# Optimization experiments

Hardware: AMD Instinct MI355X
Metric: run time of the kernel (lower is better)

The kernel has to match this reference:

```python
import jax, jax.numpy as jnp
import numpy as np

N = 100000      # nodes
R = 4           # relations
E = 500000      # edges per relation
IN, HID, OUT = 128, 128, 64


def _rel_conv(x, src, dst, W, b):
    """One DGL GraphConv (norm='both') over one relation's edge list.
    out = D_dst^{-1/2} * segsum_dst( D_src^{-1/2} x[src] ) @ W + b
    """
    ones = jnp.ones(src.shape[0], dtype=x.dtype)
    out_deg = jax.ops.segment_sum(ones, src, num_segments=N)
    in_deg = jax.ops.segment_sum(ones, dst, num_segments=N)
    norm_src = jax.lax.rsqrt(jnp.maximum(out_deg, 1.0))
    norm_dst = jax.lax.rsqrt(jnp.maximum(in_deg, 1.0))
    msg = (x * norm_src[:, None])[src]                       # [E, d] gather
    agg = jax.ops.segment_sum(msg, dst, num_segments=N)      # [N, d] scatter-add
    agg = agg * norm_dst[:, None]
    return agg @ W + b


def setup_inputs() -> dict:
    key = jax.random.key(0)
    ks = jax.random.split(key, 8)
    x = jax.random.normal(ks[0], (N, IN), dtype=jnp.float32)
    edge_src = jax.random.randint(ks[1], (R, E), 0, N, dtype=jnp.int32)
    edge_dst = jax.random.randint(ks[2], (R, E), 0, N, dtype=jnp.int32)
    s1 = 1.0 / np.sqrt(IN)
    s2 = 1.0 / np.sqrt(HID)
    W1 = jax.random.normal(ks[3], (R, IN, HID), dtype=jnp.float32) * s1
    b1 = jnp.zeros((R, HID), dtype=jnp.float32)
    W2 = jax.random.normal(ks[4], (R, HID, OUT), dtype=jnp.float32) * s2
    b2 = jnp.zeros((R, OUT), dtype=jnp.float32)
    return {"x": x, "edge_src": edge_src, "edge_dst": edge_dst,
            "W1": W1, "b1": b1, "W2": W2, "b2": b2}


def reference(x, edge_src, edge_dst, W1, b1, W2, b2):
    # layer 1: per-relation GraphConv, aggregate='sum' across relations
    h = _rel_conv(x, edge_src[0], edge_dst[0], W1[0], b1[0])
    for r in range(1, R):
        h = h + _rel_conv(x, edge_src[r], edge_dst[r], W1[r], b1[r])
    h = jax.nn.relu(h)
    # layer 2
    out = _rel_conv(h, edge_src[0], edge_dst[0], W2[0], b2[0])
    for r in range(1, R):
        out = out + _rel_conv(h, edge_src[r], edge_dst[r], W2[r], b2[r])
    return out
```

## Files before the change

kernel.cpp:

```cpp
#include <hip/hip_runtime.h>


constexpr int Nn  = 100000;
constexpr int Rr  = 4;
constexpr int Ee  = 500000;
constexpr int RE  = Rr * Ee;
constexpr int TOT = Rr * Nn;
constexpr int NP  = 100096;
constexpr int NPB = NP / 128;
constexpr int CAPN = 56;

constexpr int CB2   = (RE / 2 + 255) / 256;
constexpr int GB1   = 4 * NPB;
constexpr int PAIR1 = 2 * GB1;
constexpr int P1_GRID = PAIR1 + (CB2 - GB1) + 1;

constexpr int FB = (RE / 4 + 255) / 256;

typedef short bf16x8 __attribute__((ext_vector_type(8)));
typedef float f32x4  __attribute__((ext_vector_type(4)));

__device__ __forceinline__ unsigned short f2bf(float f) {
    unsigned u = __builtin_bit_cast(unsigned, f);
    u = u + 0x7FFFu + ((u >> 16) & 1u);
    return (unsigned short)(u >> 16);
}
__device__ __forceinline__ float bf2f(unsigned short h) {
    unsigned u = ((unsigned)h) << 16;
    return __builtin_bit_cast(float, u);
}
__device__ __forceinline__ float bfbits_lo(unsigned p) {
    return __builtin_bit_cast(float, p << 16);
}
__device__ __forceinline__ float bfbits_hi(unsigned p) {
    return __builtin_bit_cast(float, p & 0xFFFF0000u);
}

__device__ __forceinline__ void count_body2(int sub, int tid,
    const int* __restrict__ src, const int* __restrict__ dst,
    unsigned* __restrict__ deg, unsigned* __restrict__ slot)
{
    int e0 = (sub * 256 + tid) * 2;
    if (e0 >= RE) return;
    int r = (unsigned)e0 / (unsigned)Ee;
    int base = r * Nn;
    int2 s2 = *reinterpret_cast<const int2*>(src + e0);
    int2 d2 = *reinterpret_cast<const int2*>(dst + e0);
    atomicAdd(&deg[base + s2.x], 1u);
    atomicAdd(&deg[base + s2.y], 1u);
    uint2 sl;
    sl.x = atomicAdd(&deg[TOT + d2.x * Rr + r], 1u);
    sl.y = atomicAdd(&deg[TOT + d2.y * Rr + r], 1u);
    *reinterpret_cast<uint2*>(slot + e0) = sl;
}

__device__ __forceinline__ void bsum_body(int tid,
    const float* __restrict__ b1, const float* __restrict__ b2,
    float* __restrict__ bs1, float* __restrict__ bs2)
{
    if (tid < 128) bs1[tid] = b1[tid] + b1[128 + tid] + b1[256 + tid] + b1[384 + tid];
    if (tid < 64)  bs2[tid] = b2[tid] + b2[64 + tid] + b2[128 + tid] + b2[192 + tid];
}

template<int BN, bool CONVA, bool ALO>
__device__ __forceinline__ void gemm_body(
    const short* __restrict__ Xh, const short* __restrict__ Xl,
    const float* __restrict__ Xf,
    const short* __restrict__ WhT_, const short* __restrict__ WlT_,
    short* __restrict__ Y_, int CW, int rowblk, int rel)
{
    constexpr int BM = 128, BKp = 40;
    constexpr int MFR = (BN == 128) ? 4 : 2;
    constexpr int NFR = 4;
    const short* WhT = WhT_ + (size_t)rel * (BN * 128);
    const short* WlT = WlT_ + (size_t)rel * (BN * 128);
    short* Y = Y_ + (size_t)rel * BN;

    __shared__ __align__(16) short Ah[BM * BKp];
    __shared__ __align__(16) short Al[ALO ? BM * BKp : 16];
    __shared__ __align__(16) short Bh[BN * BKp], Bl[BN * BKp];

    const int tid = threadIdx.x;
    const int lane = tid & 63, wid = tid >> 6;
    const int lr = lane & 15, lg = lane >> 4;
    const int wm0 = (BN == 128) ? (wid >> 1) * 64 : wid * 32;
    const int wn0 = (BN == 128) ? (wid & 1) * 64 : 0;
    const int row0 = rowblk * BM;

    f32x4 acc[MFR][NFR];
    #pragma unroll
    for (int m = 0; m < MFR; ++m)
        #pragma unroll
        for (int n = 0; n < NFR; ++n)
            #pragma unroll
            for (int j = 0; j < 4; ++j) acc[m][n][j] = 0.f;

    const int sr = tid >> 1;
    const int sko = (tid & 1) * 16;

    for (int ks = 0; ks < 4; ++ks) {
        if constexpr (CONVA) {
            int grow = row0 + sr;
            float v[16];
            if (grow < Nn) {
                const float* xp = Xf + (size_t)grow * 128 + ks * 32 + sko;
                float4 a0 = *reinterpret_cast<const float4*>(xp);
                float4 a1 = *reinterpret_cast<const float4*>(xp + 4);
                float4 a2 = *reinterpret_cast<const float4*>(xp + 8);
                float4 a3 = *reinterpret_cast<const float4*>(xp + 12);
                v[0]=a0.x; v[1]=a0.y; v[2]=a0.z; v[3]=a0.w;
                v[4]=a1.x; v[5]=a1.y; v[6]=a1.z; v[7]=a1.w;
                v[8]=a2.x; v[9]=a2.y; v[10]=a2.z; v[11]=a2.w;
                v[12]=a3.x; v[13]=a3.y; v[14]=a3.z; v[15]=a3.w;
            } else {
                #pragma unroll
                for (int i = 0; i < 16; ++i) v[i] = 0.f;
            }
            bf16x8 h0, h1, l0, l1;
            #pragma unroll
            for (int i = 0; i < 8; ++i) {
                unsigned short h = f2bf(v[i]);
                h0[i] = (short)h; l0[i] = (short)f2bf(v[i] - bf2f(h));
                unsigned short g = f2bf(v[8 + i]);
                h1[i] = (short)g; l1[i] = (short)f2bf(v[8 + i] - bf2f(g));
            }
            *reinterpret_cast<bf16x8*>(&Ah[sr * BKp + sko])     = h0;
            *reinterpret_cast<bf16x8*>(&Ah[sr * BKp + sko + 8]) = h1;
            *reinterpret_cast<bf16x8*>(&Al[sr * BKp + sko])     = l0;
            *reinterpret_cast<bf16x8*>(&Al[sr * BKp + sko + 8]) = l1;
        } else {
            size_t ga = (size_t)(row0 + sr) * 128 + ks * 32 + sko;
            *reinterpret_cast<bf16x8*>(&Ah[sr * BKp + sko])     = *reinterpret_cast<const bf16x8*>(&Xh[ga]);
            *reinterpret_cast<bf16x8*>(&Ah[sr * BKp + sko + 8]) = *reinterpret_cast<const bf16x8*>(&Xh[ga + 8]);
            if constexpr (ALO) {
                *reinterpret_cast<bf16x8*>(&Al[sr * BKp + sko])     = *reinterpret_cast<const bf16x8*>(&Xl[ga]);
                *reinterpret_cast<bf16x8*>(&Al[sr * BKp + sko + 8]) = *reinterpret_cast<const bf16x8*>(&Xl[ga + 8]);
            }
        }
        if (BN == 128 || tid < 128) {
            size_t gb = (size_t)sr * 128 + ks * 32 + sko;
            *reinterpret_cast<bf16x8*>(&Bh[sr * BKp + sko])     = *reinterpret_cast<const bf16x8*>(&WhT[gb]);
            *reinterpret_cast<bf16x8*>(&Bh[sr * BKp + sko + 8]) = *reinterpret_cast<const bf16x8*>(&WhT[gb + 8]);
            *reinterpret_cast<bf16x8*>(&Bl[sr * BKp + sko])     = *reinterpret_cast<const bf16x8*>(&WlT[gb]);
            *reinterpret_cast<bf16x8*>(&Bl[sr * BKp + sko + 8]) = *reinterpret_cast<const bf16x8*>(&WlT[gb + 8]);
        }
        __syncthreads();

        bf16x8 bh[NFR], bl[NFR];
        #pragma unroll
        for (int n = 0; n < NFR; ++n) {
            bh[n] = *reinterpret_cast<const bf16x8*>(&Bh[(wn0 + n * 16 + lr) * BKp + lg * 8]);
            bl[n] = *reinterpret_cast<const bf16x8*>(&Bl[(wn0 + n * 16 + lr) * BKp + lg * 8]);
        }
        __builtin_amdgcn_s_setprio(1);
        #pragma unroll
        for (int m = 0; m < MFR; ++m) {
            bf16x8 ah = *reinterpret_cast<const bf16x8*>(&Ah[(wm0 + m * 16 + lr) * BKp + lg * 8]);
            #pragma unroll
            for (int n = 0; n < NFR; ++n) {
                acc[m][n] = __builtin_amdgcn_mfma_f32_16x16x32_bf16(ah, bh[n], acc[m][n], 0, 0, 0);
                acc[m][n] = __builtin_amdgcn_mfma_f32_16x16x32_bf16(ah, bl[n], acc[m][n], 0, 0, 0);
            }
            if constexpr (ALO) {
                bf16x8 al = *reinterpret_cast<const bf16x8*>(&Al[(wm0 + m * 16 + lr) * BKp + lg * 8]);
                #pragma unroll
                for (int n = 0; n < NFR; ++n)
                    acc[m][n] = __builtin_amdgcn_mfma_f32_16x16x32_bf16(al, bh[n], acc[m][n], 0, 0, 0);
            }
        }
        __builtin_amdgcn_s_setprio(0);
        __syncthreads();
    }

    #pragma unroll
    for (int m = 0; m < MFR; ++m)
        #pragma unroll
        for (int n = 0; n < NFR; ++n) {
            int col = wn0 + n * 16 + lr;
            int rb = row0 + wm0 + m * 16 + lg * 4;
            #pragma unroll
            for (int j = 0; j < 4; ++j)
                Y[(size_t)(rb + j) * CW + col] = (short)f2bf(acc[m][n][j]);
        }
}

__global__ __launch_bounds__(256)
void phase1_kernel(const int* __restrict__ src, const int* __restrict__ dst,
                   unsigned* __restrict__ deg, unsigned* __restrict__ slot,
                   const float* __restrict__ X,
                   const short* __restrict__ w1h, const short* __restrict__ w1l,
                   short* __restrict__ Y,
                   const float* __restrict__ b1, const float* __restrict__ b2,
                   float* __restrict__ bs1, float* __restrict__ bs2)
{
    int bid = blockIdx.x, tid = threadIdx.x;
    if (bid < PAIR1) {
        int sub = bid >> 1;
        if (bid & 1) {
            int rel = sub & 3, rowblk = sub >> 2;
            gemm_body<128, true, true>(nullptr, nullptr, X, w1h, w1l, Y, 512, rowblk, rel);
        } else {
            count_body2(sub, tid, src, dst, deg, slot);
        }
    } else {
        int t = bid - PAIR1;
        if (t < CB2 - GB1) count_body2(GB1 + t, tid, src, dst, deg, slot);
        else              bsum_body(tid, b1, b2, bs1, bs2);
    }
}

__global__ __launch_bounds__(256)
void count_kernel(const int* __restrict__ src, const int* __restrict__ dst,
                  unsigned* __restrict__ deg, unsigned* __restrict__ slot)
{
    count_body2(blockIdx.x, threadIdx.x, src, dst, deg, slot);
}

__global__ void bsum_kernel(const float* __restrict__ b1, const float* __restrict__ b2,
                            float* __restrict__ bs1, float* __restrict__ bs2)
{
    bsum_body(threadIdx.x, b1, b2, bs1, bs2);
}

__global__ __launch_bounds__(256)
void norms_kernel(const unsigned* __restrict__ deg, float* __restrict__ nsrc,
                  uint4* __restrict__ degq, float4* __restrict__ ndstq)
{
    int gid = blockIdx.x * 256 + threadIdx.x;
    if (gid < TOT) {
        unsigned sd = deg[gid];
        nsrc[gid] = rsqrtf((float)(sd > 0u ? sd : 1u));
    }
    if (gid < Nn) {
        uint4 dq = *reinterpret_cast<const uint4*>(deg + TOT + gid * 4);
        degq[gid] = dq;
        float4 nq;
        nq.x = rsqrtf((float)(dq.x > 0u ? dq.x : 1u));
        nq.y = rsqrtf((float)(dq.y > 0u ? dq.y : 1u));
        nq.z = rsqrtf((float)(dq.z > 0u ? dq.z : 1u));
        nq.w = rsqrtf((float)(dq.w > 0u ? dq.w : 1u));
        ndstq[gid] = nq;
    }
}

__global__ __launch_bounds__(256)
void fill_csr_kernel(const int* __restrict__ src, const int* __restrict__ dst,
                     const unsigned* __restrict__ slot, const uint4* __restrict__ degq,
                     const float4* __restrict__ ndstq, const float* __restrict__ nsrc,
                     int2* __restrict__ csrw)
{
    int e0 = (blockIdx.x * 256 + threadIdx.x) * 4;
    if (e0 >= RE) return;
    int r = (unsigned)e0 / (unsigned)Ee;
    int base = r * Nn;
    int4 s4 = *reinterpret_cast<const int4*>(src + e0);
    int4 d4 = *reinterpret_cast<const int4*>(dst + e0);
    uint4 sl = *reinterpret_cast<const uint4*>(slot + e0);
    #pragma unroll
    for (int i = 0; i < 4; ++i) {
        int s = (i == 0) ? s4.x : (i == 1) ? s4.y : (i == 2) ? s4.z : s4.w;
        int d = (i == 0) ? d4.x : (i == 1) ? d4.y : (i == 2) ? d4.z : d4.w;
        unsigned k = (i == 0) ? sl.x : (i == 1) ? sl.y : (i == 2) ? sl.z : sl.w;
        uint4 dq = degq[d];
        float4 nq = ndstq[d];
        unsigned pre = (r > 0 ? dq.x : 0u) + (r > 1 ? dq.y : 0u) + (r > 2 ? dq.z : 0u);
        float nd = (r == 0) ? nq.x : (r == 1) ? nq.y : (r == 2) ? nq.z : nq.w;
        float w = nsrc[base + s] * nd;
        unsigned pos = pre + k;
        if (pos < (unsigned)CAPN) {
            int2 v; v.x = s | (r << 17); v.y = __builtin_bit_cast(int, w);
            csrw[(size_t)d * CAPN + pos] = v;
        }
    }
}

__global__ __launch_bounds__(256)
void convw_kernel(const float* __restrict__ W1, const float* __restrict__ W2,
                  short* __restrict__ w1h, short* __restrict__ w1l,
                  short* __restrict__ w2h, short* __restrict__ w2l)
{
    int gid = blockIdx.x * 256 + threadIdx.x;
    if (gid < 4 * 128 * 128) {
        int r = gid >> 14, rem = gid & 16383, n = rem >> 7, k = rem & 127;
        float v = W1[(r << 14) + k * 128 + n];
        unsigned short h = f2bf(v);
        unsigned short l = f2bf(v - bf2f(h));
        w1h[(r << 14) + n * 128 + k] = (short)h;
        w1l[(r << 14) + n * 128 + k] = (short)l;
    } else {
        int g2 = gid - 65536;
        if (g2 >= 4 * 64 * 128) return;
        int r = g2 >> 13, rem = g2 & 8191, n = rem >> 7, k = rem & 127;
        float v = W2[(r << 13) + k * 64 + n];
        unsigned short h = f2bf(v);
        unsigned short l = f2bf(v - bf2f(h));
        w2h[(r << 13) + n * 128 + k] = (short)h;
        w2l[(r << 13) + n * 128 + k] = (short)l;
    }
}

template<int BN, bool CONVA, bool ALO>
__global__ __launch_bounds__(256)
void gemm_kernel(const short* __restrict__ Xh, const short* __restrict__ Xl,
                 const float* __restrict__ Xf,
                 const short* __restrict__ WhT_, const short* __restrict__ WlT_,
                 short* __restrict__ Y_, int CW)
{
    gemm_body<BN, CONVA, ALO>(Xh, Xl, Xf, WhT_, WlT_, Y_, CW, blockIdx.x, blockIdx.y);
}

__global__ __launch_bounds__(512)
void gemm64f_kernel(const short* __restrict__ Xh,
                    const short* __restrict__ w2h, const short* __restrict__ w2l,
                    short* __restrict__ Y)
{
    constexpr int BKp = 40;
    __shared__ __align__(16) short Ah[128 * BKp];
    __shared__ __align__(16) short Bh[256 * BKp], Bl[256 * BKp];

    const int tid = threadIdx.x;
    const int lane = tid & 63, wv = tid >> 6;
    const int rel = wv >> 1, wm0 = (wv & 1) * 64;
    const int lr = lane & 15, lg = lane >> 4;
    const int row0 = blockIdx.x * 128;

    f32x4 acc[4][4];
    #pragma unroll
    for (int m = 0; m < 4; ++m)
        #pragma unroll
        for (int n = 0; n < 4; ++n)
            #pragma unroll
            for (int j = 0; j < 4; ++j) acc[m][n][j] = 0.f;

    const int sra = tid >> 2, ska = (tid & 3) * 8;
    const int rb = tid >> 7, nb = (tid >> 1) & 63, skb = (tid & 1) * 16;

    for (int ks = 0; ks < 4; ++ks) {
        size_t ga = (size_t)(row0 + sra) * 128 + ks * 32 + ska;
        *reinterpret_cast<bf16x8*>(&Ah[sra * BKp + ska]) = *reinterpret_cast<const bf16x8*>(&Xh[ga]);
        size_t gb = (size_t)rb * (64 * 128) + (size_t)nb * 128 + ks * 32 + skb;
        *reinterpret_cast<bf16x8*>(&Bh[(rb * 64 + nb) * BKp + skb])     = *reinterpret_cast<const bf16x8*>(&w2h[gb]);
        *reinterpret_cast<bf16x8*>(&Bh[(rb * 64 + nb) * BKp + skb + 8]) = *reinterpret_cast<const bf16x8*>(&w2h[gb + 8]);
        *reinterpret_cast<bf16x8*>(&Bl[(rb * 64 + nb) * BKp + skb])     = *reinterpret_cast<const bf16x8*>(&w2l[gb]);
        *reinterpret_cast<bf16x8*>(&Bl[(rb * 64 + nb) * BKp + skb + 8]) = *reinterpret_cast<const bf16x8*>(&w2l[gb + 8]);
        __syncthreads();

        bf16x8 bh[4], bl[4];
        #pragma unroll
        for (int n = 0; n < 4; ++n) {
            bh[n] = *reinterpret_cast<const bf16x8*>(&Bh[(rel * 64 + n * 16 + lr) * BKp + lg * 8]);
            bl[n] = *reinterpret_cast<const bf16x8*>(&Bl[(rel * 64 + n * 16 + lr) * BKp + lg * 8]);
        }
        __builtin_amdgcn_s_setprio(1);
        #pragma unroll
        for (int m = 0; m < 4; ++m) {
            bf16x8 ah = *reinterpret_cast<const bf16x8*>(&Ah[(wm0 + m * 16 + lr) * BKp + lg * 8]);
            #pragma unroll
            for (int n = 0; n < 4; ++n) {
                acc[m][n] = __builtin_amdgcn_mfma_f32_16x16x32_bf16(ah, bh[n], acc[m][n], 0, 0, 0);
                acc[m][n] = __builtin_amdgcn_mfma_f32_16x16x32_bf16(ah, bl[n], acc[m][n], 0, 0, 0);
            }
        }
        __builtin_amdgcn_s_setprio(0);
        __syncthreads();
    }

    #pragma unroll
    for (int m = 0; m < 4; ++m)
        #pragma unroll
        for (int n = 0; n < 4; ++n) {
            int col = rel * 64 + n * 16 + lr;
            int rbse = row0 + wm0 + m * 16 + lg * 4;
            #pragma unroll
            for (int j = 0; j < 4; ++j)
                Y[(size_t)(rbse + j) * 256 + col] = (short)f2bf(acc[m][n][j]);
        }
}

template<int F, int NRl>
__global__ __launch_bounds__(256)
void gather_kernel(const short* __restrict__ Y, const uint4* __restrict__ degq,
                   const int2* __restrict__ csrw, const float* __restrict__ bsum,
                   float* __restrict__ H, short* __restrict__ Xh,
                   int CW, int rel, int accumulate, int finalize)
{
    constexpr int LPE = (F == 128) ? 16 : 8;
    constexpr int QN  = 64 / LPE;
    constexpr int FL  = F / LPE;
    int wid = (blockIdx.x * 256 + threadIdx.x) >> 6;
    int lane = threadIdx.x & 63;
    int q = lane / LPE, li = lane & (LPE - 1);
    if (wid >= Nn) return;

    uint4 dq = degq[wid];
    unsigned e, e1;
    if (NRl == 4) {
        unsigned tot = dq.x + dq.y + dq.z + dq.w;
        if (tot > (unsigned)CAPN) tot = CAPN;
        e = (unsigned)wid * CAPN; e1 = e + tot;
    } else {
        unsigned pre = (rel > 0 ? dq.x : 0u) + (rel > 1 ? dq.y : 0u) + (rel > 2 ? dq.z : 0u);
        unsigned len = (rel == 0) ? dq.x : (rel == 1) ? dq.y : (rel == 2) ? dq.z : dq.w;
        if (pre > (unsigned)CAPN) pre = CAPN;
        if (pre + len > (unsigned)CAPN) len = CAPN - pre;
        e = (unsigned)wid * CAPN + pre; e1 = e + len;
    }

    float t[FL];
    #pragma unroll
    for (int f = 0; f < FL; ++f) t[f] = 0.f;

    auto yaddr = [&](int2 a) -> const short* {
        int s = a.x & 0x1FFFF;
        int rl = (NRl == 4) ? ((a.x >> 17) & 3) : 0;
        return Y + (size_t)s * CW + rl * F + li * FL;
    };
    auto accum1 = [&](int2 a) {
        const short* ya = yaddr(a);
        float wa = __builtin_bit_cast(float, a.y);
        uint4 pa = *reinterpret_cast<const uint4*>(ya);
        t[0] += wa * bfbits_lo(pa.x); t[1] += wa * bfbits_hi(pa.x);
        t[2] += wa * bfbits_lo(pa.y); t[3] += wa * bfbits_hi(pa.y);
        t[4] += wa * bfbits_lo(pa.z); t[5] += wa * bfbits_hi(pa.z);
        t[6] += wa * bfbits_lo(pa.w); t[7] += wa * bfbits_hi(pa.w);
    };

    for (; e + 4 * QN <= e1; e += 4 * QN) {
        int2 a0 = csrw[e + q], a1 = csrw[e + QN + q];
        int2 a2 = csrw[e + 2 * QN + q], a3 = csrw[e + 3 * QN + q];
        const short* y0 = yaddr(a0); const short* y1 = yaddr(a1);
        const short* y2 = yaddr(a2); const short* y3 = yaddr(a3);
        float w0 = __builtin_bit_cast(float, a0.y), w1 = __builtin_bit_cast(float, a1.y);
        float w2 = __builtin_bit_cast(float, a2.y), w3 = __builtin_bit_cast(float, a3.y);
        uint4 p0 = *reinterpret_cast<const uint4*>(y0);
        uint4 p1 = *reinterpret_cast<const uint4*>(y1);
        uint4 p2 = *reinterpret_cast<const uint4*>(y2);
        uint4 p3 = *reinterpret_cast<const uint4*>(y3);
        t[0] += w0*bfbits_lo(p0.x) + w1*bfbits_lo(p1.x) + w2*bfbits_lo(p2.x) + w3*bfbits_lo(p3.x);
        t[1] += w0*bfbits_hi(p0.x) + w1*bfbits_hi(p1.x) + w2*bfbits_hi(p2.x) + w3*bfbits_hi(p3.x);
        t[2] += w0*bfbits_lo(p0.y) + w1*bfbits_lo(p1.y) + w2*bfbits_lo(p2.y) + w3*bfbits_lo(p3.y);
        t[3] += w0*bfbits_hi(p0.y) + w1*bfbits_hi(p1.y) + w2*bfbits_hi(p2.y) + w3*bfbits_hi(p3.y);
        t[4] += w0*bfbits_lo(p0.z) + w1*bfbits_lo(p1.z) + w2*bfbits_lo(p2.z) + w3*bfbits_lo(p3.z);
        t[5] += w0*bfbits_hi(p0.z) + w1*bfbits_hi(p1.z) + w2*bfbits_hi(p2.z) + w3*bfbits_hi(p3.z);
        t[6] += w0*bfbits_lo(p0.w) + w1*bfbits_lo(p1.w) + w2*bfbits_lo(p2.w) + w3*bfbits_lo(p3.w);
        t[7] += w0*bfbits_hi(p0.w) + w1*bfbits_hi(p1.w) + w2*bfbits_hi(p2.w) + w3*bfbits_hi(p3.w);
    }
    if (e + 2 * QN <= e1) {
        int2 a0 = csrw[e + q], a1 = csrw[e + QN + q];
        const short* y0 = yaddr(a0); const short* y1 = yaddr(a1);
        float w0 = __builtin_bit_cast(float, a0.y), w1 = __builtin_bit_cast(float, a1.y);
        uint4 p0 = *reinterpret_cast<const uint4*>(y0);
        uint4 p1 = *reinterpret_cast<const uint4*>(y1);
        t[0] += w0*bfbits_lo(p0.x) + w1*bfbits_lo(p1.x);
        t[1] += w0*bfbits_hi(p0.x) + w1*bfbits_hi(p1.x);
        t[2] += w0*bfbits_lo(p0.y) + w1*bfbits_lo(p1.y);
        t[3] += w0*bfbits_hi(p0.y) + w1*bfbits_hi(p1.y);
        t[4] += w0*bfbits_lo(p0.z) + w1*bfbits_lo(p1.z);
        t[5] += w0*bfbits_hi(p0.z) + w1*bfbits_hi(p1.z);
        t[6] += w0*bfbits_lo(p0.w) + w1*bfbits_lo(p1.w);
        t[7] += w0*bfbits_hi(p0.w) + w1*bfbits_hi(p1.w);
        e += 2 * QN;
    }
    if (e + QN <= e1) {
        accum1(csrw[e + q]);
        e += QN;
    }
    int nrem = (int)(e1 - e);
    if (q < nrem) accum1(csrw[e + q]);

    #pragma unroll
    for (int f = 0; f < FL; ++f) {
        #pragma unroll
        for (int o = LPE; o < 64; o <<= 1)
            t[f] += __shfl_xor(t[f], o, 64);
    }
    if (q != 0) return;

    float* hp = H + (size_t)wid * F + li * FL;
    if (accumulate) {
        #pragma unroll
        for (int f = 0; f < FL; ++f) t[f] += hp[f];
    } else {
        #pragma unroll
        for (int f = 0; f < FL; ++f) t[f] += bsum[li * FL + f];
    }
    if (F == 128 && finalize) {
        short hv[8];
        #pragma unroll
        for (int f = 0; f < FL; ++f)
            hv[f] = (short)f2bf(fmaxf(t[f], 0.f));
        *reinterpret_cast<uint4*>(Xh + (size_t)wid * F + li * FL) = *reinterpret_cast<uint4*>(hv);
    } else {
        *reinterpret_cast<float4*>(hp)     = make_float4(t[0], t[1], t[2], t[3]);
        *reinterpret_cast<float4*>(hp + 4) = make_float4(t[4], t[5], t[6], t[7]);
    }
}

extern "C" void kernel_launch(void* const* d_in, const int* in_sizes, int n_in,
                              void* d_out, int out_size, void* d_ws, size_t ws_size,
                              hipStream_t stream)
{
    const float* x  = (const float*)d_in[0];
    const int* esrc = (const int*)d_in[1];
    const int* edst = (const int*)d_in[2];
    const float* W1 = (const float*)d_in[3];
    const float* b1 = (const float*)d_in[4];
    const float* W2 = (const float*)d_in[5];
    const float* b2 = (const float*)d_in[6];
    float* out = (float*)d_out;

    char* ws = (char*)d_ws;
    size_t off = 0;
    auto alloc = [&](size_t bytes) { char* p = ws + off; off += (bytes + 255) & ~(size_t)255; return p; };
    unsigned* deg   = (unsigned*)alloc((size_t)2 * TOT * 4);
    float*    nsrc  = (float*)   alloc((size_t)TOT * 4);
    uint4*    degq  = (uint4*)   alloc((size_t)Nn * 16);
    float4*   ndstq = (float4*)  alloc((size_t)Nn * 16);
    unsigned* slot  = (unsigned*)alloc((size_t)RE * 4);
    float*    bs1   = (float*)   alloc(128 * 4);
    float*    bs2   = (float*)   alloc(64 * 4);
    short*    w1h   = (short*)   alloc((size_t)4 * 128 * 128 * 2);
    short*    w1l   = (short*)   alloc((size_t)4 * 128 * 128 * 2);
    short*    w2h   = (short*)   alloc((size_t)4 * 64 * 128 * 2);
    short*    w2l   = (short*)   alloc((size_t)4 * 64 * 128 * 2);
    int2*     csrw  = (int2*)    alloc((size_t)Nn * CAPN * 8);
    short*    xh    = (short*)   alloc((size_t)NP * 128 * 2);

    size_t yslot = (size_t)NP * 128 * 2;
    bool pathA = (ws_size >= off + 4 * yslot + 4096);
    float* h = nullptr;
    short* Y;
    if (pathA) {
        Y = (short*)alloc(4 * yslot);
    } else {
        h = (float*)alloc((size_t)NP * 128 * 4);
        Y = (short*)alloc(yslot);
    }

    const int ggrid = (Nn * 64 + 255) / 256;
    const int ngrid = (TOT + 255) / 256;

    convw_kernel<<<384, 256, 0, stream>>>(W1, W2, w1h, w1l, w2h, w2l);
    hipMemsetAsync(deg, 0, (size_t)2 * TOT * 4, stream);

    if (pathA) {
        phase1_kernel<<<P1_GRID, 256, 0, stream>>>(
            esrc, edst, deg, slot, x, w1h, w1l, Y, b1, b2, bs1, bs2);
        norms_kernel<<<ngrid, 256, 0, stream>>>(deg, nsrc, degq, ndstq);
        fill_csr_kernel<<<FB, 256, 0, stream>>>(esrc, edst, slot, degq, ndstq, nsrc, csrw);
        gather_kernel<128, 4><<<ggrid, 256, 0, stream>>>(
            Y, degq, csrw, bs1, (float*)out , xh, 512, 0, 0, 1);
        gemm64f_kernel<<<NPB, 512, 0, stream>>>(xh, w2h, w2l, Y);
        gather_kernel<64, 4><<<ggrid, 256, 0, stream>>>(
            Y, degq, csrw, bs2, out, nullptr, 256, 0, 0, 0);
    } else {
        count_kernel<<<CB2, 256, 0, stream>>>(esrc, edst, deg, slot);
        bsum_kernel<<<1, 128, 0, stream>>>(b1, b2, bs1, bs2);
        norms_kernel<<<ngrid, 256, 0, stream>>>(deg, nsrc, degq, ndstq);
        fill_csr_kernel<<<FB, 256, 0, stream>>>(esrc, edst, slot, degq, ndstq, nsrc, csrw);
        for (int r = 0; r < Rr; ++r) {
            gemm_kernel<128, true, true><<<dim3(NPB, 1), 256, 0, stream>>>(
                nullptr, nullptr, x, w1h + (size_t)r * 128 * 128, w1l + (size_t)r * 128 * 128, Y, 128);
            gather_kernel<128, 1><<<ggrid, 256, 0, stream>>>(
                Y, degq, csrw, bs1, h, xh, 128, r, r > 0, r == Rr - 1);
        }
        for (int r = 0; r < Rr; ++r) {
            gemm_kernel<64, false, false><<<dim3(NPB, 1), 256, 0, stream>>>(
                xh, nullptr, nullptr, w2h + (size_t)r * 64 * 128, w2l + (size_t)r * 64 * 128, Y, 64);
            gather_kernel<64, 1><<<ggrid, 256, 0, stream>>>(
                Y, degq, csrw, bs2, out, nullptr, 64, r, r > 0, 0);
        }
    }
}
```

Before: 386.9 us.

## Fuse layer-1 gather with layer-2 GEMM and drop norms kernel

Removes the separate norms kernel: fill_csr now computes rsqrt of the source and destination degrees inline from the raw degree array, and gather reads the in-degree quads directly. It also adds a fused kernel that gathers the layer-1 aggregate for 128 rows into shared memory, applies bias and ReLU, and immediately runs the layer-2 MFMA GEMM. This avoids writing and re-reading the bf16 hidden matrix and saves kernel launches. In exchange it uses a large shared-memory footprint, which lowers occupancy for the latency-bound gather phase, and it needs a separate Y2 buffer when the workspace is large enough.

```diff
diff --git a/kernel.cpp b/kernel.cpp
--- a/kernel.cpp
+++ b/kernel.cpp
@@ -34,6 +34,9 @@
 }
 __device__ __forceinline__ float bfbits_hi(unsigned p) {
     return __builtin_bit_cast(float, p & 0xFFFF0000u);
+}
+__device__ __forceinline__ float rsq(unsigned d) {
+    return rsqrtf((float)(d > 0u ? d : 1u));
 }
 
 __device__ __forceinline__ void count_body2(int sub, int tid,
@@ -223,30 +226,8 @@
 }
 
 __global__ __launch_bounds__(256)
-void norms_kernel(const unsigned* __restrict__ deg, float* __restrict__ nsrc,
-                  uint4* __restrict__ degq, float4* __restrict__ ndstq)
-{
-    int gid = blockIdx.x * 256 + threadIdx.x;
-    if (gid < TOT) {
-        unsigned sd = deg[gid];
-        nsrc[gid] = rsqrtf((float)(sd > 0u ? sd : 1u));
-    }
-    if (gid < Nn) {
-        uint4 dq = *reinterpret_cast<const uint4*>(deg + TOT + gid * 4);
-        degq[gid] = dq;
-        float4 nq;
-        nq.x = rsqrtf((float)(dq.x > 0u ? dq.x : 1u));
-        nq.y = rsqrtf((float)(dq.y > 0u ? dq.y : 1u));
-        nq.z = rsqrtf((float)(dq.z > 0u ? dq.z : 1u));
-        nq.w = rsqrtf((float)(dq.w > 0u ? dq.w : 1u));
-        ndstq[gid] = nq;
-    }
-}
-
-__global__ __launch_bounds__(256)
 void fill_csr_kernel(const int* __restrict__ src, const int* __restrict__ dst,
-                     const unsigned* __restrict__ slot, const uint4* __restrict__ degq,
-                     const float4* __restrict__ ndstq, const float* __restrict__ nsrc,
+                     const unsigned* __restrict__ slot, const unsigned* __restrict__ deg,
                      int2* __restrict__ csrw)
 {
     int e0 = (blockIdx.x * 256 + threadIdx.x) * 4;
@@ -261,11 +242,10 @@
         int s = (i == 0) ? s4.x : (i == 1) ? s4.y : (i == 2) ? s4.z : s4.w;
         int d = (i == 0) ? d4.x : (i == 1) ? d4.y : (i == 2) ? d4.z : d4.w;
         unsigned k = (i == 0) ? sl.x : (i == 1) ? sl.y : (i == 2) ? sl.z : sl.w;
-        uint4 dq = degq[d];
-        float4 nq = ndstq[d];
+        uint4 dq = *reinterpret_cast<const uint4*>(deg + TOT + d * 4);
         unsigned pre = (r > 0 ? dq.x : 0u) + (r > 1 ? dq.y : 0u) + (r > 2 ? dq.z : 0u);
-        float nd = (r == 0) ? nq.x : (r == 1) ? nq.y : (r == 2) ? nq.z : nq.w;
-        float w = nsrc[base + s] * nd;
+        unsigned dr = (r == 0) ? dq.x : (r == 1) ? dq.y : (r == 2) ? dq.z : dq.w;
+        float w = rsq(deg[base + s]) * rsq(dr);
         unsigned pos = pre + k;
         if (pos < (unsigned)CAPN) {
             int2 v; v.x = s | (r << 17); v.y = __builtin_bit_cast(int, w);
@@ -377,9 +357,162 @@
         }
 }
 
+__global__ __launch_bounds__(512)
+void fuse2_kernel(const short* __restrict__ Y1, const unsigned* __restrict__ deg,
+                  const int2* __restrict__ csrw, const float* __restrict__ bs1,
+                  const short* __restrict__ w2h, const short* __restrict__ w2l,
+                  short* __restrict__ Y2)
+{
+    constexpr int BKp = 40;
+    __shared__ __align__(16) short AhF[4 * 128 * BKp];
+    __shared__ __align__(16) short Bh[256 * BKp], Bl[256 * BKp];
+
+    const int tid = threadIdx.x;
+    const int lane = tid & 63, wv = tid >> 6;
+    const int q = lane >> 4, li = lane & 15;
+    const int row0 = blockIdx.x * 128;
+
+    for (int i = 0; i < 16; ++i) {
+        int ln = wv * 16 + i;
+        int wid = row0 + ln;
+        float t[8];
+        #pragma unroll
+        for (int f = 0; f < 8; ++f) t[f] = 0.f;
+
+        if (wid < Nn) {
+            uint4 dq = *reinterpret_cast<const uint4*>(deg + TOT + wid * 4);
+            unsigned tot = dq.x + dq.y + dq.z + dq.w;
+            if (tot > (unsigned)CAPN) tot = CAPN;
+            unsigned e = (unsigned)wid * CAPN, e1 = e + tot;
+
+            auto yaddr = [&](int2 a) -> const short* {
+                int s = a.x & 0x1FFFF;
+                int rl = (a.x >> 17) & 3;
+                return Y1 + (size_t)s * 512 + rl * 128 + li * 8;
+            };
+            auto acc1 = [&](int2 a) {
+                const short* ya = yaddr(a);
+                float wa = __builtin_bit_cast(float, a.y);
+                uint4 pa = *reinterpret_cast<const uint4*>(ya);
+                t[0] += wa * bfbits_lo(pa.x); t[1] += wa * bfbits_hi(pa.x);
+                t[2] += wa * bfbits_lo(pa.y); t[3] += wa * bfbits_hi(pa.y);
+                t[4] += wa * bfbits_lo(pa.z); t[5] += wa * bfbits_hi(pa.z);
+                t[6] += wa * bfbits_lo(pa.w); t[7] += wa * bfbits_hi(pa.w);
+            };
+
+            for (; e + 16 <= e1; e += 16) {
+                int2 a0 = csrw[e + q], a1 = csrw[e + 4 + q];
+                int2 a2 = csrw[e + 8 + q], a3 = csrw[e + 12 + q];
+                const short* y0 = yaddr(a0); const short* y1 = yaddr(a1);
+                const short* y2 = yaddr(a2); const short* y3 = yaddr(a3);
+                float w0 = __builtin_bit_cast(float, a0.y), w1 = __builtin_bit_cast(float, a1.y);
+                float w2 = __builtin_bit_cast(float, a2.y), w3 = __builtin_bit_cast(float, a3.y);
+                uint4 p0 = *reinterpret_cast<const uint4*>(y0);
+                uint4 p1 = *reinterpret_cast<const uint4*>(y1);
+                uint4 p2 = *reinterpret_cast<const uint4*>(y2);
+                uint4 p3 = *reinterpret_cast<const uint4*>(y3);
+                t[0] += w0*bfbits_lo(p0.x) + w1*bfbits_lo(p1.x) + w2*bfbits_lo(p2.x) + w3*bfbits_lo(p3.x);
+                t[1] += w0*bfbits_hi(p0.x) + w1*bfbits_hi(p1.x) + w2*bfbits_hi(p2.x) + w3*bfbits_hi(p3.x);
+                t[2] += w0*bfbits_lo(p0.y) + w1*bfbits_lo(p1.y) + w2*bfbits_lo(p2.y) + w3*bfbits_lo(p3.y);
+                t[3] += w0*bfbits_hi(p0.y) + w1*bfbits_hi(p1.y) + w2*bfbits_hi(p2.y) + w3*bfbits_hi(p3.y);
+                t[4] += w0*bfbits_lo(p0.z) + w1*bfbits_lo(p1.z) + w2*bfbits_lo(p2.z) + w3*bfbits_lo(p3.z);
+                t[5] += w0*bfbits_hi(p0.z) + w1*bfbits_hi(p1.z) + w2*bfbits_hi(p2.z) + w3*bfbits_hi(p3.z);
+                t[6] += w0*bfbits_lo(p0.w) + w1*bfbits_lo(p1.w) + w2*bfbits_lo(p2.w) + w3*bfbits_lo(p3.w);
+                t[7] += w0*bfbits_hi(p0.w) + w1*bfbits_hi(p1.w) + w2*bfbits_hi(p2.w) + w3*bfbits_hi(p3.w);
+            }
+            if (e + 8 <= e1) {
+                int2 a0 = csrw[e + q], a1 = csrw[e + 4 + q];
+                const short* y0 = yaddr(a0); const short* y1 = yaddr(a1);
+                float w0 = __builtin_bit_cast(float, a0.y), w1 = __builtin_bit_cast(float, a1.y);
+                uint4 p0 = *reinterpret_cast<const uint4*>(y0);
+                uint4 p1 = *reinterpret_cast<const uint4*>(y1);
+                t[0] += w0*bfbits_lo(p0.x) + w1*bfbits_lo(p1.x);
+                t[1] += w0*bfbits_hi(p0.x) + w1*bfbits_hi(p1.x);
+                t[2] += w0*bfbits_lo(p0.y) + w1*bfbits_lo(p1.y);
+                t[3] += w0*bfbits_hi(p0.y) + w1*bfbits_hi(p1.y);
+                t[4] += w0*bfbits_lo(p0.z) + w1*bfbits_lo(p1.z);
+                t[5] += w0*bfbits_hi(p0.z) + w1*bfbits_hi(p1.z);
+                t[6] += w0*bfbits_lo(p0.w) + w1*bfbits_lo(p1.w);
+                t[7] += w0*bfbits_hi(p0.w) + w1*bfbits_hi(p1.w);
+                e += 8;
+            }
+            if (e + 4 <= e1) { acc1(csrw[e + q]); e += 4; }
+            int nrem = (int)(e1 - e);
+            if (q < nrem) acc1(csrw[e + q]);
+        }
+
+        #pragma unroll
+        for (int f = 0; f < 8; ++f) {
+            t[f] += __shfl_xor(t[f], 16, 64);
+            t[f] += __shfl_xor(t[f], 32, 64);
+        }
+        if (q == 0) {
+            short hv[8];
+            #pragma unroll
+            for (int f = 0; f < 8; ++f)
+                hv[f] = (short)f2bf(fmaxf(t[f] + bs1[li * 8 + f], 0.f));
+            *reinterpret_cast<uint4*>(&AhF[(li >> 2) * (128 * BKp) + ln * BKp + (li & 3) * 8])
+                = *reinterpret_cast<uint4*>(hv);
+        }
+    }
+    __syncthreads();
+
+    const int rel = wv >> 1, wm0 = (wv & 1) * 64;
+    const int lr = lane & 15, lg = lane >> 4;
+    f32x4 acc[4][4];
+    #pragma unroll
+    for (int m = 0; m < 4; ++m)
+        #pragma unroll
+        for (int n = 0; n < 4; ++n)
+            #pragma unroll
+            for (int j = 0; j < 4; ++j) acc[m][n][j] = 0.f;
+
+    const int rb = tid >> 7, nb = (tid >> 1) & 63, skb = (tid & 1) * 16;
+
+    for (int ks = 0; ks < 4; ++ks) {
+        size_t gb = (size_t)rb * (64 * 128) + (size_t)nb * 128 + ks * 32 + skb;
+        *reinterpret_cast<bf16x8*>(&Bh[(rb * 64 + nb) * BKp + skb])     = *reinterpret_cast<const bf16x8*>(&w2h[gb]);
+        *reinterpret_cast<bf16x8*>(&Bh[(rb * 64 + nb) * BKp + skb + 8]) = *reinterpret_cast<const bf16x8*>(&w2h[gb + 8]);
+        *reinterpret_cast<bf16x8*>(&Bl[(rb * 64 + nb) * BKp + skb])     = *reinterpret_cast<const bf16x8*>(&w2l[gb]);
+        *reinterpret_cast<bf16x8*>(&Bl[(rb * 64 + nb) * BKp + skb + 8]) = *reinterpret_cast<const bf16x8*>(&w2l[gb + 8]);
+        __syncthreads();
+
+        bf16x8 bh[4], bl[4];
+        #pragma unroll
+        for (int n = 0; n < 4; ++n) {
+            bh[n] = *reinterpret_cast<const bf16x8*>(&Bh[(rel * 64 + n * 16 + lr) * BKp + lg * 8]);
+            bl[n] = *reinterpret_cast<const bf16x8*>(&Bl[(rel * 64 + n * 16 + lr) * BKp + lg * 8]);
+        }
+        __builtin_amdgcn_s_setprio(1);
+        #pragma unroll
+        for (int m = 0; m < 4; ++m) {
+            bf16x8 ah = *reinterpret_cast<const bf16x8*>(
+                &AhF[ks * (128 * BKp) + (wm0 + m * 16 + lr) * BKp + lg * 8]);
+            #pragma unroll
+            for (int n = 0; n < 4; ++n) {
+                acc[m][n] = __builtin_amdgcn_mfma_f32_16x16x32_bf16(ah, bh[n], acc[m][n], 0, 0, 0);
+                acc[m][n] = __builtin_amdgcn_mfma_f32_16x16x32_bf16(ah, bl[n], acc[m][n], 0, 0, 0);
+            }
+        }
+        __builtin_amdgcn_s_setprio(0);
+        __syncthreads();
+    }
+
+    #pragma unroll
+    for (int m = 0; m < 4; ++m)
+        #pragma unroll
+        for (int n = 0; n < 4; ++n) {
+            int col = rel * 64 + n * 16 + lr;
+            int rbse = row0 + wm0 + m * 16 + lg * 4;
+            #pragma unroll
+            for (int j = 0; j < 4; ++j)
+                Y2[(size_t)(rbse + j) * 256 + col] = (short)f2bf(acc[m][n][j]);
+        }
+}
+
 template<int F, int NRl>
 __global__ __launch_bounds__(256)
-void gather_kernel(const short* __restrict__ Y, const uint4* __restrict__ degq,
+void gather_kernel(const short* __restrict__ Y, const unsigned* __restrict__ deg,
                    const int2* __restrict__ csrw, const float* __restrict__ bsum,
                    float* __restrict__ H, short* __restrict__ Xh,
                    int CW, int rel, int accumulate, int finalize)
@@ -392,7 +525,7 @@
     int q = lane / LPE, li = lane & (LPE - 1);
     if (wid >= Nn) return;
 
-    uint4 dq = degq[wid];
+    uint4 dq = *reinterpret_cast<const uint4*>(deg + TOT + wid * 4);
     unsigned e, e1;
     if (NRl == 4) {
         unsigned tot = dq.x + dq.y + dq.z + dq.w;
@@ -461,10 +594,7 @@
         t[7] += w0*bfbits_hi(p0.w) + w1*bfbits_hi(p1.w);
         e += 2 * QN;
     }
-    if (e + QN <= e1) {
-        accum1(csrw[e + q]);
-        e += QN;
-    }
+    if (e + QN <= e1) { accum1(csrw[e + q]); e += QN; }
     int nrem = (int)(e1 - e);
     if (q < nrem) accum1(csrw[e + q]);
 
@@ -512,63 +642,63 @@
     char* ws = (char*)d_ws;
     size_t off = 0;
     auto alloc = [&](size_t bytes) { char* p = ws + off; off += (bytes + 255) & ~(size_t)255; return p; };
-    unsigned* deg   = (unsigned*)alloc((size_t)2 * TOT * 4);
-    float*    nsrc  = (float*)   alloc((size_t)TOT * 4);
-    uint4*    degq  = (uint4*)   alloc((size_t)Nn * 16);
-    float4*   ndstq = (float4*)  alloc((size_t)Nn * 16);
-    unsigned* slot  = (unsigned*)alloc((size_t)RE * 4);
-    float*    bs1   = (float*)   alloc(128 * 4);
-    float*    bs2   = (float*)   alloc(64 * 4);
-    short*    w1h   = (short*)   alloc((size_t)4 * 128 * 128 * 2);
-    short*    w1l   = (short*)   alloc((size_t)4 * 128 * 128 * 2);
-    short*    w2h   = (short*)   alloc((size_t)4 * 64 * 128 * 2);
-    short*    w2l   = (short*)   alloc((size_t)4 * 64 * 128 * 2);
-    int2*     csrw  = (int2*)    alloc((size_t)Nn * CAPN * 8);
-    short*    xh    = (short*)   alloc((size_t)NP * 128 * 2);
+    unsigned* deg  = (unsigned*)alloc((size_t)2 * TOT * 4);
+    unsigned* slot = (unsigned*)alloc((size_t)RE * 4);
+    float*    bs1  = (float*)   alloc(128 * 4);
+    float*    bs2  = (float*)   alloc(64 * 4);
+    short*    w1h  = (short*)   alloc((size_t)4 * 128 * 128 * 2);
+    short*    w1l  = (short*)   alloc((size_t)4 * 128 * 128 * 2);
+    short*    w2h  = (short*)   alloc((size_t)4 * 64 * 128 * 2);
+    short*    w2l  = (short*)   alloc((size_t)4 * 64 * 128 * 2);
+    int2*     csrw = (int2*)    alloc((size_t)Nn * CAPN * 8);
+    short*    xh   = (short*)   alloc((size_t)NP * 128 * 2);
 
     size_t yslot = (size_t)NP * 128 * 2;
     bool pathA = (ws_size >= off + 4 * yslot + 4096);
     float* h = nullptr;
-    short* Y;
+    short* Y1;
     if (pathA) {
-        Y = (short*)alloc(4 * yslot);
+        Y1 = (short*)alloc(4 * yslot);
     } else {
-        h = (float*)alloc((size_t)NP * 128 * 4);
-        Y = (short*)alloc(yslot);
-    }
+        h  = (float*)alloc((size_t)NP * 128 * 4);
+        Y1 = (short*)alloc(yslot);
+    }
+    bool fused = pathA && (ws_size >= off + 2 * yslot + 4096);
+    short* Y2 = fused ? (short*)alloc(2 * yslot) : Y1;
 
     const int ggrid = (Nn * 64 + 255) / 256;
-    const int ngrid = (TOT + 255) / 256;
 
     convw_kernel<<<384, 256, 0, stream>>>(W1, W2, w1h, w1l, w2h, w2l);
     hipMemsetAsync(deg, 0, (size_t)2 * TOT * 4, stream);
 
     if (pathA) {
         phase1_kernel<<<P1_GRID, 256, 0, stream>>>(
-            esrc, edst, deg, slot, x, w1h, w1l, Y, b1, b2, bs1, bs2);
-        norms_kernel<<<ngrid, 256, 0, stream>>>(deg, nsrc, degq, ndstq);
-        fill_csr_kernel<<<FB, 256, 0, stream>>>(esrc, edst, slot, degq, ndstq, nsrc, csrw);
-        gather_kernel<128, 4><<<ggrid, 256, 0, stream>>>(
-            Y, degq, csrw, bs1, (float*)out , xh, 512, 0, 0, 1);
-        gemm64f_kernel<<<NPB, 512, 0, stream>>>(xh, w2h, w2l, Y);
+            esrc, edst, deg, slot, x, w1h, w1l, Y1, b1, b2, bs1, bs2);
+        fill_csr_kernel<<<FB, 256, 0, stream>>>(esrc, edst, slot, deg, csrw);
+        if (fused) {
+            fuse2_kernel<<<NPB, 512, 0, stream>>>(Y1, deg, csrw, bs1, w2h, w2l, Y2);
+        } else {
+            gather_kernel<128, 4><<<ggrid, 256, 0, stream>>>(
+                Y1, deg, csrw, bs1, (float*)out , xh, 512, 0, 0, 1);
+            gemm64f_kernel<<<NPB, 512, 0, stream>>>(xh, w2h, w2l, Y2);
+        }
         gather_kernel<64, 4><<<ggrid, 256, 0, stream>>>(
-            Y, degq, csrw, bs2, out, nullptr, 256, 0, 0, 0);
+            Y2, deg, csrw, bs2, out, nullptr, 256, 0, 0, 0);
     } else {
         count_kernel<<<CB2, 256, 0, stream>>>(esrc, edst, deg, slot);
         bsum_kernel<<<1, 128, 0, stream>>>(b1, b2, bs1, bs2);
-        norms_kernel<<<ngrid, 256, 0, stream>>>(deg, nsrc, degq, ndstq);
-        fill_csr_kernel<<<FB, 256, 0, stream>>>(esrc, edst, slot, degq, ndstq, nsrc, csrw);
+        fill_csr_kernel<<<FB, 256, 0, stream>>>(esrc, edst, slot, deg, csrw);
         for (int r = 0; r < Rr; ++r) {
             gemm_kernel<128, true, true><<<dim3(NPB, 1), 256, 0, stream>>>(
-                nullptr, nullptr, x, w1h + (size_t)r * 128 * 128, w1l + (size_t)r * 128 * 128, Y, 128);
+                nullptr, nullptr, x, w1h + (size_t)r * 128 * 128, w1l + (size_t)r * 128 * 128, Y1, 128);
             gather_kernel<128, 1><<<ggrid, 256, 0, stream>>>(
-                Y, degq, csrw, bs1, h, xh, 128, r, r > 0, r == Rr - 1);
+                Y1, deg, csrw, bs1, h, xh, 128, r, r > 0, r == Rr - 1);
         }
         for (int r = 0; r < Rr; ++r) {
             gemm_kernel<64, false, false><<<dim3(NPB, 1), 256, 0, stream>>>(
-                xh, nullptr, nullptr, w2h + (size_t)r * 64 * 128, w2l + (size_t)r * 64 * 128, Y, 64);
+                xh, nullptr, nullptr, w2h + (size_t)r * 64 * 128, w2l + (size_t)r * 64 * 128, Y1, 64);
             gather_kernel<64, 1><<<ggrid, 256, 0, stream>>>(
-                Y, degq, csrw, bs2, out, nullptr, 64, r, r > 0, 0);
-        }
-    }
-}
+                Y1, deg, csrw, bs2, out, nullptr, 64, r, r > 0, 0);
+        }
+    }
+}
```

New measurement: 410.0 us. 6.0% more time.
